# Optimization experiments

Hardware: AMD Instinct MI355X
Metric: run time of the kernel (lower is better)

The kernel has to match this reference:

```python
import jax, jax.numpy as jnp
import numpy as np

N = 100000
E = 800000
IN_CH = 128
HID = 32
HEADS = 8
OUT_CH = 40
NEG_SLOPE = 0.2


def setup_inputs() -> dict:
    key = jax.random.key(0)
    ks = jax.random.split(key, 10)
    x = jax.random.normal(ks[0], (N, IN_CH), dtype=jnp.float32)
    edge_index = jax.random.randint(ks[1], (2, E), 0, N, dtype=jnp.int64)
    # GATConv layer 1: in -> heads*hid, concat=True
    s1 = 1.0 / np.sqrt(IN_CH)
    W1 = jax.random.uniform(ks[2], (IN_CH, HEADS * HID), jnp.float32, -s1, s1)
    att_src1 = jax.random.uniform(ks[3], (1, HEADS, HID), jnp.float32, -s1, s1)
    att_dst1 = jax.random.uniform(ks[4], (1, HEADS, HID), jnp.float32, -s1, s1)
    b1 = jnp.zeros((HEADS * HID,), jnp.float32)
    # GATConv layer 2: heads*hid -> out, heads=1, concat=True
    s2 = 1.0 / np.sqrt(HEADS * HID)
    W2 = jax.random.uniform(ks[5], (HEADS * HID, OUT_CH), jnp.float32, -s2, s2)
    att_src2 = jax.random.uniform(ks[6], (1, 1, OUT_CH), jnp.float32, -s2, s2)
    att_dst2 = jax.random.uniform(ks[7], (1, 1, OUT_CH), jnp.float32, -s2, s2)
    b2 = jnp.zeros((OUT_CH,), jnp.float32)
    return {"x": x, "edge_index": edge_index,
            "W1": W1, "att_src1": att_src1, "att_dst1": att_dst1, "b1": b1,
            "W2": W2, "att_src2": att_src2, "att_dst2": att_dst2, "b2": b2}


def _gat_layer(x, src, dst, W, att_src, att_dst, bias, heads, out_ch):
    n = x.shape[0]
    xp = (x @ W).reshape(n, heads, out_ch)               # [N,H,C]
    a_src = jnp.sum(xp * att_src, axis=-1)               # [N,H]
    a_dst = jnp.sum(xp * att_dst, axis=-1)               # [N,H]
    logits = a_src[src] + a_dst[dst]                      # [Etot,H]
    logits = jnp.where(logits > 0, logits, NEG_SLOPE * logits)  # leaky_relu
    # segment softmax over destination node
    m = jax.ops.segment_max(logits, dst, num_segments=n)  # [N,H]
    p = jnp.exp(logits - m[dst])
    z = jax.ops.segment_sum(p, dst, num_segments=n)
    alpha = p / (z[dst] + 1e-16)                           # [Etot,H]
    out = jax.ops.segment_sum(xp[src] * alpha[:, :, None], dst, num_segments=n)
    return out.reshape(n, heads * out_ch) + bias


def reference(x, edge_index, W1, att_src1, att_dst1, b1, W2, att_src2, att_dst2, b2):
    n = x.shape[0]
    # add self loops (PyG GATConv default add_self_loops=True)
    loop = jnp.arange(n, dtype=edge_index.dtype)
    src = jnp.concatenate([edge_index[0], loop])
    dst = jnp.concatenate([edge_index[1], loop])
    # dropout p=0.2 is identity in eval mode
    h = _gat_layer(x, src, dst, W1, att_src1, att_dst1, b1, HEADS, HID)
    h = jax.nn.relu(h)
    out = _gat_layer(h, src, dst, W2, att_src2, att_dst2, b2, 1, OUT_CH)
    return jax.nn.log_softmax(out, axis=1)
```

## Files before the change

kernel.cpp:

```cpp
#include <hip/hip_runtime.h>
#include <math.h>

#define NN 100000
#define NE 800000
#define C1 256
#define OC 40
#define XPAD 64
#define NEG 0.2f

typedef _Float16 h4 __attribute__((ext_vector_type(4)));
typedef _Float16 h8 __attribute__((ext_vector_type(8)));
typedef float f4v __attribute__((ext_vector_type(4)));
typedef float f2v __attribute__((ext_vector_type(2)));

static __device__ __forceinline__ float leaky(float v){ return v > 0.f ? v : NEG*v; }

static __device__ __forceinline__ h8 cvt8(const float4* p){
  float4 a = p[0], b = p[1];
  h8 r = {(_Float16)a.x,(_Float16)a.y,(_Float16)a.z,(_Float16)a.w,
          (_Float16)b.x,(_Float16)b.y,(_Float16)b.z,(_Float16)b.w};
  return r;
}


__global__ __launch_bounds__(256) void k_wt(const float* __restrict__ W1, const float* __restrict__ W2,
                                            _Float16* __restrict__ W1t, _Float16* __restrict__ W2t){
  int b = blockIdx.x;
  if (b < 128){
    int k = b, nb = threadIdx.x;
    W1t[(size_t)nb*128 + k] = (_Float16)W1[k*256 + nb];
  } else {
    int nb = b - 128;
    int e = threadIdx.x;
    int l = e >> 2, j = e & 3;
    int k = (l>>5)*128 + ((l>>4)&1)*64 + j*16 + (l&15);
    float v = (nb < OC) ? W2[(size_t)k*OC + nb] : 0.f;
    W2t[(size_t)nb*256 + e] = (_Float16)v;
  }
}

__global__ __launch_bounds__(256) void k_gemm1(const float* __restrict__ x,
    const _Float16* __restrict__ W1t, const float* __restrict__ attS,
    const float* __restrict__ attD, unsigned* __restrict__ xp1w,
    float* __restrict__ asrc, float* __restrict__ adst)
{
  const int tid  = threadIdx.x;
  const int lane = tid & 63;
  const int w    = tid >> 6;
  const int wr = w >> 1, wc = w & 1;
  const int n = lane & 15, quad = lane >> 4;
  const int r0 = blockIdx.x * 64;

  float aSc[8], aDc[8];
  #pragma unroll
  for (int ct = 0; ct < 8; ++ct){
    int col = wc*128 + ct*16 + n;
    aSc[ct] = attS[col]; aDc[ct] = attD[col];
  }

  f4v acc[2][8];
  #pragma unroll
  for (int rt = 0; rt < 2; ++rt)
    #pragma unroll
    for (int ct = 0; ct < 8; ++ct) acc[rt][ct] = (f4v){0.f,0.f,0.f,0.f};

  const int row0 = r0 + wr*32 + n;
  const int ra = (row0      < NN) ? row0      : NN-1;
  const int rb = (row0 + 16 < NN) ? row0 + 16 : NN-1;

  #pragma unroll
  for (int ks = 0; ks < 4; ++ks){
    h8 a0 = cvt8((const float4*)(x + (size_t)ra*128 + ks*32 + quad*8));
    h8 a1 = cvt8((const float4*)(x + (size_t)rb*128 + ks*32 + quad*8));
    #pragma unroll
    for (int ct = 0; ct < 8; ++ct){
      h8 b = *(const h8*)(W1t + (size_t)(wc*128 + ct*16 + n)*128 + ks*32 + quad*8);
      acc[0][ct] = __builtin_amdgcn_mfma_f32_16x16x32_f16(a0, b, acc[0][ct], 0, 0, 0);
      acc[1][ct] = __builtin_amdgcn_mfma_f32_16x16x32_f16(a1, b, acc[1][ct], 0, 0, 0);
    }
  }

  #pragma unroll
  for (int rt = 0; rt < 2; ++rt){
    #pragma unroll
    for (int reg = 0; reg < 4; ++reg){
      const int row = r0 + wr*32 + rt*16 + quad*4 + reg;
      const bool ok = row < NN;
      float v[8];
      #pragma unroll
      for (int ct = 0; ct < 8; ++ct) v[ct] = acc[rt][ct][reg];
      if (ok){
        unsigned dwA = (unsigned)__builtin_amdgcn_cvt_pk_fp8_f32(v[0], v[1], 0, false);
        dwA = (unsigned)__builtin_amdgcn_cvt_pk_fp8_f32(v[2], v[3], (int)dwA, true);
        unsigned dwB = (unsigned)__builtin_amdgcn_cvt_pk_fp8_f32(v[4], v[5], 0, false);
        dwB = (unsigned)__builtin_amdgcn_cvt_pk_fp8_f32(v[6], v[7], (int)dwB, true);
        unsigned* xr = xp1w + (size_t)row*64 + wc*32 + n;
        xr[0]  = dwA;
        xr[16] = dwB;
      }
      float s[4], d[4];
      #pragma unroll
      for (int h = 0; h < 4; ++h){
        s[h] = v[2*h]*aSc[2*h] + v[2*h+1]*aSc[2*h+1];
        d[h] = v[2*h]*aDc[2*h] + v[2*h+1]*aDc[2*h+1];
      }
      #pragma unroll
      for (int off = 1; off < 16; off <<= 1){
        #pragma unroll
        for (int h = 0; h < 4; ++h){
          s[h] += __shfl_xor(s[h], off, 64);
          d[h] += __shfl_xor(d[h], off, 64);
        }
      }
      if (ok && n == 0){
        #pragma unroll
        for (int h = 0; h < 4; ++h){
          asrc[row*8 + wc*4 + h] = s[h];
          adst[row*8 + wc*4 + h] = d[h];
        }
      }
    }
  }
}

__global__ __launch_bounds__(256) void k_deg_init(int* deg){
  int i = blockIdx.x*256 + threadIdx.x;
  if (i < NN) deg[i] = 1;
}
__global__ __launch_bounds__(256) void k_deg_count(const int* __restrict__ ei, int* deg){
  int i = blockIdx.x*256 + threadIdx.x;
  if (i < NE) atomicAdd(&deg[ei[NE + i]], 1);
}
__global__ __launch_bounds__(256) void k_scan1(const int* __restrict__ deg, int* part, int* bsum){
  __shared__ int lds[256];
  const int t = threadIdx.x;
  const int base = blockIdx.x*1024;
  int v[4]; int s = 0;
  #pragma unroll
  for (int i = 0; i < 4; ++i){ int idx = base + t*4 + i; v[i] = (idx < NN) ? deg[idx] : 0; s += v[i]; }
  lds[t] = s; __syncthreads();
  for (int off = 1; off < 256; off <<= 1){
    int xx = (t >= off) ? lds[t-off] : 0;
    __syncthreads();
    lds[t] += xx;
    __syncthreads();
  }
  int excl = lds[t] - s;
  #pragma unroll
  for (int i = 0; i < 4; ++i){ int idx = base + t*4 + i; if (idx < NN) part[idx] = excl; excl += v[i]; }
  if (t == 255) bsum[blockIdx.x] = lds[255];
}
__global__ void k_scan2(const int* __restrict__ bsum, int* boff){
  const int l = threadIdx.x;
  int a = (l      < 98) ? bsum[l]      : 0;
  int b = (64 + l < 98) ? bsum[64 + l] : 0;
  int sa = a, sb = b;
  #pragma unroll
  for (int off = 1; off < 64; off <<= 1){
    int ta = __shfl_up(sa, off, 64);
    int tb = __shfl_up(sb, off, 64);
    if (l >= off){ sa += ta; sb += tb; }
  }
  const int totalA = __shfl(sa, 63, 64);
  if (l      < 98) boff[l]      = sa - a;
  if (64 + l < 98) boff[64 + l] = totalA + sb - b;
}
__global__ __launch_bounds__(256) void k_scan3(const int* __restrict__ part, const int* __restrict__ boff,
                                               int* rowptr, int* cursor){
  int i = blockIdx.x*256 + threadIdx.x;
  if (i < NN){ int v = part[i] + boff[i >> 10]; rowptr[i] = v; cursor[i] = v; }
  if (i == 0) rowptr[NN] = NN + NE;
}
__global__ __launch_bounds__(256) void k_fill(const int* __restrict__ ei, int* cursor, int* __restrict__ esrc){
  int i = blockIdx.x*256 + threadIdx.x;
  if (i < NE + NN){
    int s, d;
    if (i < NE){ s = ei[i]; d = ei[NE + i]; } else { s = d = i - NE; }
    int slot = atomicAdd(&cursor[d], 1);
    esrc[slot] = s;
  }
}

template<int B>
static __device__ __forceinline__ void agg1_batch(
    const int j0, const int je, const int lane,
    const int* __restrict__ esrc, const float* __restrict__ asrc,
    const float adA, const float adB,
    const unsigned* __restrict__ xp1w,
    f2v& accLo, f2v& accHi, float& z0, float& z1)
{
  const int cnt = je - j0;
  const int slot = lane & 15;
  const int hA = (lane >> 4) << 1;
  int idx = j0 + slot; idx = idx < je ? idx : je - 1;
  const int sv = esrc[idx];
  float pv0 = 0.f, pv1 = 0.f;
  if (slot < cnt){
    f2v av = *(const f2v*)(asrc + (size_t)sv*8 + hA);
    pv0 = __expf(leaky(av.x + adA));
    pv1 = __expf(leaky(av.y + adB));
  }
  z0 += pv0; z1 += pv1;
  unsigned u[B];
  #pragma unroll
  for (int e = 0; e < B; ++e){
    int s = __builtin_amdgcn_readlane(sv, e);
    u[e] = xp1w[(size_t)s*64 + lane];
  }
  __builtin_amdgcn_sched_barrier(0);
  const int pb = lane & 48;
  #pragma unroll
  for (int e = 0; e < B; ++e){
    const float pA = __shfl(pv0, pb | e, 64);
    const float pB = __shfl(pv1, pb | e, 64);
    f2v lo = __builtin_amdgcn_cvt_pk_f32_fp8((int)u[e], false);
    f2v hi = __builtin_amdgcn_cvt_pk_f32_fp8((int)u[e], true);
    accLo += (f2v){pA, pA} * lo;
    accHi += (f2v){pB, pB} * hi;
  }
}

__global__ __launch_bounds__(256) void k_agg1(const unsigned* __restrict__ xp1w,
    const float* __restrict__ asrc, const float* __restrict__ adst,
    const float* __restrict__ b1, const int* __restrict__ rowptr,
    const int* __restrict__ esrc, _Float16* __restrict__ h1)
{
  const int lane = threadIdx.x & 63;
  int n = __builtin_amdgcn_readfirstlane(blockIdx.x*4 + (threadIdx.x >> 6));
  const int hA = (lane >> 4) << 1;
  const f2v ad = *(const f2v*)(adst + (size_t)n*8 + hA);
  const int jb = rowptr[n], je = rowptr[n+1];
  const int cbase = (lane>>5)*128 + ((lane>>4)&1)*64 + (lane&15);
  const float bp0 = b1[cbase], bp1 = b1[cbase+16], bp2 = b1[cbase+32], bp3 = b1[cbase+48];
  f2v accLo = {0.f,0.f}, accHi = {0.f,0.f};
  float z0 = 0.f, z1 = 0.f;

  int j0 = jb;
  while (j0 < je){
    if (je - j0 > 8){
      agg1_batch<16>(j0, je, lane, esrc, asrc, ad.x, ad.y, xp1w, accLo, accHi, z0, z1);
      j0 += 16;
    } else {
      agg1_batch<8>(j0, je, lane, esrc, asrc, ad.x, ad.y, xp1w, accLo, accHi, z0, z1);
      j0 += 8;
    }
  }
  #pragma unroll
  for (int off = 1; off <= 8; off <<= 1){
    z0 += __shfl_xor(z0, off, 64);
    z1 += __shfl_xor(z1, off, 64);
  }
  const float invA = 1.f/(z0 + 1e-16f), invB = 1.f/(z1 + 1e-16f);
  h4 o = {(_Float16)fmaxf(accLo.x*invA + bp0, 0.f),
          (_Float16)fmaxf(accLo.y*invA + bp1, 0.f),
          (_Float16)fmaxf(accHi.x*invB + bp2, 0.f),
          (_Float16)fmaxf(accHi.y*invB + bp3, 0.f)};
  ((h4*)h1)[(size_t)n*64 + lane] = o;
}

__global__ __launch_bounds__(256) void k_gemm2(const _Float16* __restrict__ h1,
    const _Float16* __restrict__ W2t, const float* __restrict__ attS,
    const float* __restrict__ attD, _Float16* __restrict__ xp2,
    float* __restrict__ asrc2, float* __restrict__ adst2)
{
  const int tid  = threadIdx.x;
  const int lane = tid & 63;
  const int w    = tid >> 6;
  const int n = lane & 15, quad = lane >> 4;
  const int r0 = blockIdx.x * 256 + w*64;

  float aSc[3], aDc[3];
  #pragma unroll
  for (int ct = 0; ct < 3; ++ct){
    int col = ct*16 + n;
    aSc[ct] = (col < OC) ? attS[col] : 0.f;
    aDc[ct] = (col < OC) ? attD[col] : 0.f;
  }

  f4v acc[4][3];
  #pragma unroll
  for (int rt = 0; rt < 4; ++rt)
    #pragma unroll
    for (int ct = 0; ct < 3; ++ct) acc[rt][ct] = (f4v){0.f,0.f,0.f,0.f};

  int rr[4];
  #pragma unroll
  for (int rt = 0; rt < 4; ++rt){
    int r = r0 + rt*16 + n;
    rr[rt] = (r < NN) ? r : NN-1;
  }

  #pragma unroll
  for (int ks = 0; ks < 8; ++ks){
    h8 b[3];
    #pragma unroll
    for (int ct = 0; ct < 3; ++ct)
      b[ct] = *(const h8*)(W2t + (size_t)(ct*16 + n)*256 + ks*32 + quad*8);
    #pragma unroll
    for (int rt = 0; rt < 4; ++rt){
      h8 a = *(const h8*)(h1 + (size_t)rr[rt]*256 + ks*32 + quad*8);
      #pragma unroll
      for (int ct = 0; ct < 3; ++ct)
        acc[rt][ct] = __builtin_amdgcn_mfma_f32_16x16x32_f16(a, b[ct], acc[rt][ct], 0, 0, 0);
    }
  }

  #pragma unroll
  for (int rt = 0; rt < 4; ++rt){
    #pragma unroll
    for (int reg = 0; reg < 4; ++reg){
      const int row = r0 + rt*16 + quad*4 + reg;
      const bool ok = row < NN;
      float v0 = acc[rt][0][reg], v1 = acc[rt][1][reg], v2 = acc[rt][2][reg];
      float s = v0*aSc[0] + v1*aSc[1] + v2*aSc[2];
      float d = v0*aDc[0] + v1*aDc[1] + v2*aDc[2];
      #pragma unroll
      for (int off = 1; off < 16; off <<= 1){
        s += __shfl_xor(s, off, 64);
        d += __shfl_xor(d, off, 64);
      }
      if (ok){
        _Float16* xr = xp2 + (size_t)row*XPAD + n;
        xr[0]  = (_Float16)v0;
        xr[16] = (_Float16)v1;
        if (n < 8) xr[32] = (_Float16)v2;
        if (n == 0){ asrc2[row] = s; adst2[row] = d; }
      }
    }
  }
}

__global__ __launch_bounds__(256) void k_agg2(const _Float16* __restrict__ xp2,
    const float* __restrict__ asrc2, const float* __restrict__ adst2,
    const float* __restrict__ b2, const int* __restrict__ rowptr,
    const int* __restrict__ esrc, float* __restrict__ out)
{
  const int lane = threadIdx.x & 63;
  int n = __builtin_amdgcn_readfirstlane(blockIdx.x*4 + (threadIdx.x >> 6));
  const float ad = adst2[n];
  const int jb = rowptr[n], je = rowptr[n+1];
  const bool act = lane < OC;
  float acc = 0.f, zacc = 0.f;

  for (int j0 = jb; j0 < je; j0 += 16) {
    const int cnt = je - j0;
    int idx = j0 + (lane & 15); idx = idx < je ? idx : je - 1;
    const int sv = esrc[idx];
    const float pv = (lane < cnt && lane < 16)
                   ? __expf(leaky(asrc2[sv] + ad)) : 0.f;
    zacc += pv;
    _Float16 u[16];
    #pragma unroll
    for (int e = 0; e < 16; ++e){
      int s = __builtin_amdgcn_readlane(sv, e);
      u[e] = xp2[(size_t)s*XPAD + lane];
    }
    __builtin_amdgcn_sched_barrier(0);
    #pragma unroll
    for (int e = 0; e < 16; ++e){
      const float p = __shfl(pv, e, 64);
      acc += p * (float)u[e];
    }
  }
  #pragma unroll
  for (int off = 1; off < 64; off <<= 1) zacc += __shfl_xor(zacc, off, 64);

  float val = act ? (acc/(zacc + 1e-16f) + b2[lane]) : -INFINITY;
  float m = val;
  #pragma unroll
  for (int off = 32; off > 0; off >>= 1) m = fmaxf(m, __shfl_xor(m, off, 64));
  float e = act ? __expf(val - m) : 0.f;
  float sum = e;
  #pragma unroll
  for (int off = 32; off > 0; off >>= 1) sum += __shfl_xor(sum, off, 64);
  if (act) out[(size_t)n*OC + lane] = val - m - __logf(sum);
}

extern "C" void kernel_launch(void* const* d_in, const int* in_sizes, int n_in,
                              void* d_out, int out_size, void* d_ws, size_t ws_size,
                              hipStream_t stream)
{
  const float* x   = (const float*)d_in[0];
  const int*   ei  = (const int*)  d_in[1];
  const float* W1  = (const float*)d_in[2];
  const float* aS1 = (const float*)d_in[3];
  const float* aD1 = (const float*)d_in[4];
  const float* b1  = (const float*)d_in[5];
  const float* W2  = (const float*)d_in[6];
  const float* aS2 = (const float*)d_in[7];
  const float* aD2 = (const float*)d_in[8];
  const float* b2  = (const float*)d_in[9];
  float* out = (float*)d_out;

  char* wsp = (char*)d_ws;
  size_t off = 0;
  auto alloc = [&](size_t bytes){ void* p = wsp + off; off += (bytes + 255) & ~(size_t)255; return p; };
  unsigned* xp1w = (unsigned*)alloc((size_t)NN*C1);
  _Float16* h1  = (_Float16*)alloc((size_t)NN*C1*2);
  float* as1  = (float*)alloc((size_t)NN*8*4);
  float* ad1  = (float*)alloc((size_t)NN*8*4);
  float* as2  = (float*)alloc((size_t)NN*4);
  float* ad2  = (float*)alloc((size_t)NN*4);
  int* deg    = (int*)alloc((size_t)NN*4);
  int* part   = (int*)alloc((size_t)NN*4);
  int* rowptr = (int*)alloc((size_t)(NN+1)*4);
  int* cursor = (int*)alloc((size_t)NN*4);
  int* bsum   = (int*)alloc(98*4);
  int* boff   = (int*)alloc(98*4);
  int* esrc   = (int*)alloc((size_t)(NN+NE)*4);
  _Float16* W1t = (_Float16*)alloc((size_t)256*128*2);
  _Float16* W2t = (_Float16*)alloc((size_t)48*256*2);
  _Float16* xp2 = (_Float16*)alloc((size_t)NN*XPAD*2);
  (void)ws_size; (void)in_sizes; (void)n_in; (void)out_size;

  k_wt       <<<176,  256, 0, stream>>>(W1, W2, W1t, W2t);
  k_gemm1    <<<1563, 256, 0, stream>>>(x, W1t, aS1, aD1, xp1w, as1, ad1);
  k_deg_init <<<391,  256, 0, stream>>>(deg);
  k_deg_count<<<3125, 256, 0, stream>>>(ei, deg);
  k_scan1    <<<98,   256, 0, stream>>>(deg, part, bsum);
  k_scan2    <<<1,    64,  0, stream>>>(bsum, boff);
  k_scan3    <<<391,  256, 0, stream>>>(part, boff, rowptr, cursor);
  k_fill     <<<3516, 256, 0, stream>>>(ei, cursor, esrc);
  k_agg1     <<<25000,256, 0, stream>>>(xp1w, as1, ad1, b1, rowptr, esrc, h1);
  k_gemm2    <<<391,  256, 0, stream>>>(h1, W2t, aS2, aD2, xp2, as2, ad2);
  k_agg2     <<<25000,256, 0, stream>>>(xp2, as2, ad2, b2, rowptr, esrc, out);
}
```

Before: 359.2 us.

## Fold attention vectors into weight matrices and stage x tiles through LDS

Precomputes W·att_src and W·att_dst as extra weight columns so the attention logits come straight out of the MFMA, replacing the per-row shuffle reductions in both GEMM kernels. gemm1 now loads its x tile into swizzled LDS with global_load_lds and preloads the first k-slice of B. gemm2 is restructured to one 16-row tile per wave across 4 column tiles, launched with more blocks. The cost is an extra MFMA column tile and attention logits computed from fp16-rounded folded weights, which may shift numerics slightly.

```diff
diff --git a/kernel.cpp b/kernel.cpp
--- a/kernel.cpp
+++ b/kernel.cpp
@@ -15,35 +15,62 @@
 
 static __device__ __forceinline__ float leaky(float v){ return v > 0.f ? v : NEG*v; }
 
-static __device__ __forceinline__ h8 cvt8(const float4* p){
-  float4 a = p[0], b = p[1];
+static __device__ __forceinline__ h8 mk8(float4 a, float4 b){
   h8 r = {(_Float16)a.x,(_Float16)a.y,(_Float16)a.z,(_Float16)a.w,
           (_Float16)b.x,(_Float16)b.y,(_Float16)b.z,(_Float16)b.w};
   return r;
 }
 
+static __device__ __forceinline__ void gload_lds16(const float* g, float* l){
+  __builtin_amdgcn_global_load_lds((const __attribute__((address_space(1))) void*)g,
+                                   (__attribute__((address_space(3))) void*)l, 16, 0, 0);
+}
+
 
 __global__ __launch_bounds__(256) void k_wt(const float* __restrict__ W1, const float* __restrict__ W2,
+                                            const float* __restrict__ aS1, const float* __restrict__ aD1,
+                                            const float* __restrict__ aS2, const float* __restrict__ aD2,
                                             _Float16* __restrict__ W1t, _Float16* __restrict__ W2t){
   int b = blockIdx.x;
   if (b < 128){
     int k = b, nb = threadIdx.x;
     W1t[(size_t)nb*128 + k] = (_Float16)W1[k*256 + nb];
-  } else {
+  } else if (b < 176){
     int nb = b - 128;
     int e = threadIdx.x;
     int l = e >> 2, j = e & 3;
     int k = (l>>5)*128 + ((l>>4)&1)*64 + j*16 + (l&15);
     float v = (nb < OC) ? W2[(size_t)k*OC + nb] : 0.f;
     W2t[(size_t)nb*256 + e] = (_Float16)v;
+  } else if (b < 178){
+    int b2 = b - 176;
+    int h  = threadIdx.x >> 5;
+    int kb = (threadIdx.x & 31) * 4;
+    const float* att = b2 ? aD1 : aS1;
+    #pragma unroll
+    for (int kk = 0; kk < 4; ++kk){
+      int k = kb + kk;
+      float s = 0.f;
+      for (int c = 0; c < 32; ++c) s += W1[k*256 + h*32 + c] * att[h*32 + c];
+      W1t[(size_t)(256 + b2*8 + h)*128 + k] = (_Float16)s;
+    }
+  } else {
+    int j = b - 178;
+    int e = threadIdx.x;
+    int l = e >> 2, jj = e & 3;
+    int k = (l>>5)*128 + ((l>>4)&1)*64 + jj*16 + (l&15);
+    float v = 0.f;
+    if (j == 0){ for (int c = 0; c < OC; ++c) v += W2[(size_t)k*OC + c] * aS2[c]; }
+    else if (j == 1){ for (int c = 0; c < OC; ++c) v += W2[(size_t)k*OC + c] * aD2[c]; }
+    W2t[(size_t)(48 + j)*256 + e] = (_Float16)v;
   }
 }
 
 __global__ __launch_bounds__(256) void k_gemm1(const float* __restrict__ x,
-    const _Float16* __restrict__ W1t, const float* __restrict__ attS,
-    const float* __restrict__ attD, unsigned* __restrict__ xp1w,
+    const _Float16* __restrict__ W1t, unsigned* __restrict__ xp1w,
     float* __restrict__ asrc, float* __restrict__ adst)
 {
+  __shared__ float xs[64*128];
   const int tid  = threadIdx.x;
   const int lane = tid & 63;
   const int w    = tid >> 6;
@@ -51,33 +78,65 @@
   const int n = lane & 15, quad = lane >> 4;
   const int r0 = blockIdx.x * 64;
 
-  float aSc[8], aDc[8];
-  #pragma unroll
-  for (int ct = 0; ct < 8; ++ct){
-    int col = wc*128 + ct*16 + n;
-    aSc[ct] = attS[col]; aDc[ct] = attD[col];
-  }
+  if (r0 + 64 <= NN){
+    #pragma unroll
+    for (int it = 0; it < 8; ++it){
+      int idx = it*256 + tid;
+      int row = idx >> 5, c16 = idx & 31;
+      const float* src = x + (size_t)(r0 + row)*128 + ((c16 ^ (row & 7)) << 2);
+      gload_lds16(src, xs + ((size_t)(it*256 + w*64) << 2));
+    }
+  } else {
+    #pragma unroll
+    for (int it = 0; it < 8; ++it){
+      int idx = it*256 + tid;
+      int row = idx >> 5, c16 = idx & 31;
+      int gr = r0 + row; gr = gr < NN ? gr : NN-1;
+      ((float4*)xs)[idx] = *(const float4*)(x + (size_t)gr*128 + ((c16 ^ (row & 7)) << 2));
+    }
+  }
+
+  h8 b0[9];
+  #pragma unroll
+  for (int ct = 0; ct < 8; ++ct)
+    b0[ct] = *(const h8*)(W1t + (size_t)(wc*128 + ct*16 + n)*128 + quad*8);
+  if (wc == 0) b0[8] = *(const h8*)(W1t + (size_t)(256 + n)*128 + quad*8);
+
+  __syncthreads();
 
   f4v acc[2][8];
   #pragma unroll
   for (int rt = 0; rt < 2; ++rt)
     #pragma unroll
     for (int ct = 0; ct < 8; ++ct) acc[rt][ct] = (f4v){0.f,0.f,0.f,0.f};
-
-  const int row0 = r0 + wr*32 + n;
-  const int ra = (row0      < NN) ? row0      : NN-1;
-  const int rb = (row0 + 16 < NN) ? row0 + 16 : NN-1;
+  f4v accE0 = {0.f,0.f,0.f,0.f}, accE1 = {0.f,0.f,0.f,0.f};
+
+  const int rowA = wr*32 + n;
+  const int rowB = rowA + 16;
+  const int s = n & 7;
 
   #pragma unroll
   for (int ks = 0; ks < 4; ++ks){
-    h8 a0 = cvt8((const float4*)(x + (size_t)ra*128 + ks*32 + quad*8));
-    h8 a1 = cvt8((const float4*)(x + (size_t)rb*128 + ks*32 + quad*8));
+    const int base16 = ks*8 + quad*2;
+    float4 fa0 = ((const float4*)xs)[rowA*32 + ((base16    ) ^ s)];
+    float4 fa1 = ((const float4*)xs)[rowA*32 + ((base16 + 1) ^ s)];
+    float4 fb0 = ((const float4*)xs)[rowB*32 + ((base16    ) ^ s)];
+    float4 fb1 = ((const float4*)xs)[rowB*32 + ((base16 + 1) ^ s)];
+    h8 a0 = mk8(fa0, fa1);
+    h8 a1 = mk8(fb0, fb1);
     #pragma unroll
     for (int ct = 0; ct < 8; ++ct){
-      h8 b = *(const h8*)(W1t + (size_t)(wc*128 + ct*16 + n)*128 + ks*32 + quad*8);
+      h8 b = (ks == 0) ? b0[ct]
+           : *(const h8*)(W1t + (size_t)(wc*128 + ct*16 + n)*128 + ks*32 + quad*8);
       acc[0][ct] = __builtin_amdgcn_mfma_f32_16x16x32_f16(a0, b, acc[0][ct], 0, 0, 0);
       acc[1][ct] = __builtin_amdgcn_mfma_f32_16x16x32_f16(a1, b, acc[1][ct], 0, 0, 0);
     }
+    if (wc == 0){
+      h8 b = (ks == 0) ? b0[8]
+           : *(const h8*)(W1t + (size_t)(256 + n)*128 + ks*32 + quad*8);
+      accE0 = __builtin_amdgcn_mfma_f32_16x16x32_f16(a0, b, accE0, 0, 0, 0);
+      accE1 = __builtin_amdgcn_mfma_f32_16x16x32_f16(a1, b, accE1, 0, 0, 0);
+    }
   }
 
   #pragma unroll
@@ -85,11 +144,10 @@
     #pragma unroll
     for (int reg = 0; reg < 4; ++reg){
       const int row = r0 + wr*32 + rt*16 + quad*4 + reg;
-      const bool ok = row < NN;
-      float v[8];
-      #pragma unroll
-      for (int ct = 0; ct < 8; ++ct) v[ct] = acc[rt][ct][reg];
-      if (ok){
+      if (row < NN){
+        float v[8];
+        #pragma unroll
+        for (int ct = 0; ct < 8; ++ct) v[ct] = acc[rt][ct][reg];
         unsigned dwA = (unsigned)__builtin_amdgcn_cvt_pk_fp8_f32(v[0], v[1], 0, false);
         dwA = (unsigned)__builtin_amdgcn_cvt_pk_fp8_f32(v[2], v[3], (int)dwA, true);
         unsigned dwB = (unsigned)__builtin_amdgcn_cvt_pk_fp8_f32(v[4], v[5], 0, false);
@@ -97,26 +155,10 @@
         unsigned* xr = xp1w + (size_t)row*64 + wc*32 + n;
         xr[0]  = dwA;
         xr[16] = dwB;
-      }
-      float s[4], d[4];
-      #pragma unroll
-      for (int h = 0; h < 4; ++h){
-        s[h] = v[2*h]*aSc[2*h] + v[2*h+1]*aSc[2*h+1];
-        d[h] = v[2*h]*aDc[2*h] + v[2*h+1]*aDc[2*h+1];
-      }
-      #pragma unroll
-      for (int off = 1; off < 16; off <<= 1){
-        #pragma unroll
-        for (int h = 0; h < 4; ++h){
-          s[h] += __shfl_xor(s[h], off, 64);
-          d[h] += __shfl_xor(d[h], off, 64);
-        }
-      }
-      if (ok && n == 0){
-        #pragma unroll
-        for (int h = 0; h < 4; ++h){
-          asrc[row*8 + wc*4 + h] = s[h];
-          adst[row*8 + wc*4 + h] = d[h];
+        if (wc == 0){
+          float vE = (rt == 0) ? accE0[reg] : accE1[reg];
+          if (n < 8) asrc[row*8 + n] = vE;
+          else       adst[row*8 + (n - 8)] = vE;
         }
       }
     }
@@ -259,73 +301,42 @@
 }
 
 __global__ __launch_bounds__(256) void k_gemm2(const _Float16* __restrict__ h1,
-    const _Float16* __restrict__ W2t, const float* __restrict__ attS,
-    const float* __restrict__ attD, _Float16* __restrict__ xp2,
+    const _Float16* __restrict__ W2t, _Float16* __restrict__ xp2,
     float* __restrict__ asrc2, float* __restrict__ adst2)
 {
   const int tid  = threadIdx.x;
   const int lane = tid & 63;
   const int w    = tid >> 6;
   const int n = lane & 15, quad = lane >> 4;
-  const int r0 = blockIdx.x * 256 + w*64;
-
-  float aSc[3], aDc[3];
-  #pragma unroll
-  for (int ct = 0; ct < 3; ++ct){
-    int col = ct*16 + n;
-    aSc[ct] = (col < OC) ? attS[col] : 0.f;
-    aDc[ct] = (col < OC) ? attD[col] : 0.f;
-  }
-
-  f4v acc[4][3];
-  #pragma unroll
-  for (int rt = 0; rt < 4; ++rt)
-    #pragma unroll
-    for (int ct = 0; ct < 3; ++ct) acc[rt][ct] = (f4v){0.f,0.f,0.f,0.f};
-
-  int rr[4];
-  #pragma unroll
-  for (int rt = 0; rt < 4; ++rt){
-    int r = r0 + rt*16 + n;
-    rr[rt] = (r < NN) ? r : NN-1;
-  }
+  const int r0 = blockIdx.x * 64 + w*16;
+
+  f4v acc[4];
+  #pragma unroll
+  for (int ct = 0; ct < 4; ++ct) acc[ct] = (f4v){0.f,0.f,0.f,0.f};
+
+  int rr = r0 + n; rr = rr < NN ? rr : NN-1;
 
   #pragma unroll
   for (int ks = 0; ks < 8; ++ks){
-    h8 b[3];
-    #pragma unroll
-    for (int ct = 0; ct < 3; ++ct)
-      b[ct] = *(const h8*)(W2t + (size_t)(ct*16 + n)*256 + ks*32 + quad*8);
-    #pragma unroll
-    for (int rt = 0; rt < 4; ++rt){
-      h8 a = *(const h8*)(h1 + (size_t)rr[rt]*256 + ks*32 + quad*8);
-      #pragma unroll
-      for (int ct = 0; ct < 3; ++ct)
-        acc[rt][ct] = __builtin_amdgcn_mfma_f32_16x16x32_f16(a, b[ct], acc[rt][ct], 0, 0, 0);
-    }
-  }
-
-  #pragma unroll
-  for (int rt = 0; rt < 4; ++rt){
-    #pragma unroll
-    for (int reg = 0; reg < 4; ++reg){
-      const int row = r0 + rt*16 + quad*4 + reg;
-      const bool ok = row < NN;
-      float v0 = acc[rt][0][reg], v1 = acc[rt][1][reg], v2 = acc[rt][2][reg];
-      float s = v0*aSc[0] + v1*aSc[1] + v2*aSc[2];
-      float d = v0*aDc[0] + v1*aDc[1] + v2*aDc[2];
-      #pragma unroll
-      for (int off = 1; off < 16; off <<= 1){
-        s += __shfl_xor(s, off, 64);
-        d += __shfl_xor(d, off, 64);
-      }
-      if (ok){
-        _Float16* xr = xp2 + (size_t)row*XPAD + n;
-        xr[0]  = (_Float16)v0;
-        xr[16] = (_Float16)v1;
-        if (n < 8) xr[32] = (_Float16)v2;
-        if (n == 0){ asrc2[row] = s; adst2[row] = d; }
-      }
+    h8 a = *(const h8*)(h1 + (size_t)rr*256 + ks*32 + quad*8);
+    #pragma unroll
+    for (int ct = 0; ct < 4; ++ct){
+      h8 b = *(const h8*)(W2t + (size_t)(ct*16 + n)*256 + ks*32 + quad*8);
+      acc[ct] = __builtin_amdgcn_mfma_f32_16x16x32_f16(a, b, acc[ct], 0, 0, 0);
+    }
+  }
+
+  #pragma unroll
+  for (int reg = 0; reg < 4; ++reg){
+    const int row = r0 + quad*4 + reg;
+    if (row < NN){
+      float v0 = acc[0][reg], v1 = acc[1][reg], v2 = acc[2][reg], v3 = acc[3][reg];
+      _Float16* xr = xp2 + (size_t)row*XPAD + n;
+      xr[0]  = (_Float16)v0;
+      xr[16] = (_Float16)v1;
+      if (n < 8) xr[32] = (_Float16)v2;
+      if (n == 0) asrc2[row] = v3;
+      if (n == 1) adst2[row] = v3;
     }
   }
 }
@@ -408,13 +419,13 @@
   int* bsum   = (int*)alloc(98*4);
   int* boff   = (int*)alloc(98*4);
   int* esrc   = (int*)alloc((size_t)(NN+NE)*4);
-  _Float16* W1t = (_Float16*)alloc((size_t)256*128*2);
-  _Float16* W2t = (_Float16*)alloc((size_t)48*256*2);
+  _Float16* W1t = (_Float16*)alloc((size_t)272*128*2);
+  _Float16* W2t = (_Float16*)alloc((size_t)64*256*2);
   _Float16* xp2 = (_Float16*)alloc((size_t)NN*XPAD*2);
   (void)ws_size; (void)in_sizes; (void)n_in; (void)out_size;
 
-  k_wt       <<<176,  256, 0, stream>>>(W1, W2, W1t, W2t);
-  k_gemm1    <<<1563, 256, 0, stream>>>(x, W1t, aS1, aD1, xp1w, as1, ad1);
+  k_wt       <<<194,  256, 0, stream>>>(W1, W2, aS1, aD1, aS2, aD2, W1t, W2t);
+  k_gemm1    <<<1563, 256, 0, stream>>>(x, W1t, xp1w, as1, ad1);
   k_deg_init <<<391,  256, 0, stream>>>(deg);
   k_deg_count<<<3125, 256, 0, stream>>>(ei, deg);
   k_scan1    <<<98,   256, 0, stream>>>(deg, part, bsum);
@@ -422,6 +433,6 @@
   k_scan3    <<<391,  256, 0, stream>>>(part, boff, rowptr, cursor);
   k_fill     <<<3516, 256, 0, stream>>>(ei, cursor, esrc);
   k_agg1     <<<25000,256, 0, stream>>>(xp1w, as1, ad1, b1, rowptr, esrc, h1);
-  k_gemm2    <<<391,  256, 0, stream>>>(h1, W2t, aS2, aD2, xp2, as2, ad2);
+  k_gemm2    <<<1563, 256, 0, stream>>>(h1, W2t, xp2, as2, ad2);
   k_agg2     <<<25000,256, 0, stream>>>(xp2, as2, ad2, b2, rowptr, esrc, out);
 }
```

After: 364.4 us. About the same (+1.4%).
